# Kernel optimization log

Hardware: AMD Instinct MI355X
Metric: run time of the kernel (lower is better)

Reference implementation:

```python
import jax, jax.numpy as jnp
import numpy as np
from jax import lax

NUM_LAYERS = 128
SEQ_LEN = 256
H = 1  # hidden_size = input_size = 1


def setup_inputs() -> dict:
    key = jax.random.key(0)
    k = jax.random.split(key, 5)
    # PyTorch GRU init: U(-1/sqrt(H), 1/sqrt(H)) with H=1 -> U(-1, 1)
    u = lambda kk, shp: jax.random.uniform(kk, shp, jnp.float32, -1.0, 1.0)
    return {
        "x": jax.random.normal(k[0], (1, SEQ_LEN), jnp.float32),
        "w_ih": u(k[1], (NUM_LAYERS, 3 * H, H)),  # gates stacked [r, z, n]
        "w_hh": u(k[2], (NUM_LAYERS, 3 * H, H)),
        "b_ih": u(k[3], (NUM_LAYERS, 3 * H)),
        "b_hh": u(k[4], (NUM_LAYERS, 3 * H)),
    }


def _gru_stack(x_seq, w_ih, w_hh, b_ih, b_hh):
    # x_seq: [T, H]; params stacked over layers. PyTorch GRU equations, gate order r,z,n.
    def layer_step(seq, params):
        wi, wh, bi, bh = params  # [3H,H], [3H,H], [3H], [3H]

        def cell(h, xt):  # h: [H], xt: [H]
            gi = wi @ xt + bi  # [3H]
            gh = wh @ h + bh   # [3H]
            r = jax.nn.sigmoid(gi[0:H] + gh[0:H])
            z = jax.nn.sigmoid(gi[H:2 * H] + gh[H:2 * H])
            n = jnp.tanh(gi[2 * H:] + r * gh[2 * H:])
            h_new = (1.0 - z) * n + z * h
            return h_new, h_new

        h0 = jnp.zeros((H,), dtype=seq.dtype)
        _, out = lax.scan(cell, h0, seq)  # out: [T, H]
        return out, None

    out, _ = lax.scan(layer_step, x_seq, (w_ih, w_hh, b_ih, b_hh))
    return out


def reference(x, w_ih, w_hh, b_ih, b_hh):
    # x: [1, T] -> GRU input [T, H=1] (unbatched), encoder only (decoder unused in forward)
    seq = x.T  # [T, 1]
    out = _gru_stack(seq, w_ih, w_hh, b_ih, b_hh)  # [T, 1]
    return out.T  # [1, T]
```

## Files before the change

kernel.cpp:

```cpp
#include <hip/hip_runtime.h>

#define T_LEN 256
#define NG 25

__device__ __forceinline__ float ex2(float x) { return __builtin_amdgcn_exp2f(x); }
__device__ __forceinline__ float rcpf_(float x) { return __builtin_amdgcn_rcpf(x); }

__device__ __forceinline__ float dpp_shr1_fill(float fill, float v) {
    int f = __float_as_int(fill), i = __float_as_int(v);
    return __int_as_float(__builtin_amdgcn_update_dpp(f, i, 0x138, 0xF, 0xF, false));
}
__device__ __forceinline__ float dpp_shl1_fill(float fill, float v) {
    int f = __float_as_int(fill), i = __float_as_int(v);
    return __int_as_float(__builtin_amdgcn_update_dpp(f, i, 0x130, 0xF, 0xF, false));
}

__global__ __launch_bounds__(128, 1) void gru_stack_wavefront(
    const float* __restrict__ x,
    const float* __restrict__ w_ih,
    const float* __restrict__ w_hh,
    const float* __restrict__ b_ih,
    const float* __restrict__ b_hh,
    float* __restrict__ out)
{
    __shared__ float ring[2 * 64];
    __shared__ float sx[T_LEN];
    const int tid  = threadIdx.x;
    const int lane = tid & 63;
    const int wid  = tid >> 6;

    ring[tid] = 0.0f;
    sx[tid] = x[tid];
    sx[tid + 128] = x[tid + 128];

    const float L1 = -1.4426950408889634f;
    const float L2 = -2.8853900817779268f;

    const float wi_r = L1 * w_ih[3 * tid + 0], wh_r = L1 * w_hh[3 * tid + 0];
    const float b_r  = L1 * (b_ih[3 * tid + 0] + b_hh[3 * tid + 0]);
    const float wi_z = L1 * w_ih[3 * tid + 1], wh_z = L1 * w_hh[3 * tid + 1];
    const float b_z  = L1 * (b_ih[3 * tid + 1] + b_hh[3 * tid + 1]);
    const float wi_n = L2 * w_ih[3 * tid + 2], bi_n = L2 * b_ih[3 * tid + 2];
    const float wh_n = L2 * w_hh[3 * tid + 2], bh_n = L2 * b_hh[3 * tid + 2];

    float h = 0.0f;
    float c_r = b_r, c_z = b_z, g_n = bh_n;

    float pk[16];
    #pragma unroll
    for (int k = 0; k < 16; ++k) pk[k] = 0.0f;

    float ov = 0.0f;
    int t = -lane - 80 * wid - 1;

    const bool is_w1 = (wid == 1);
    float* ringw = &ring[wid * 64];

    __syncthreads();

    for (int g = 0; g < 9; ++g) {
        if (is_w1) {
            const int base = 16 * g - 17;
            #pragma unroll
            for (int k = 0; k < 16; ++k)
                pk[k] = ring[(base + k) & 63];
        } else {
            #pragma unroll
            for (int k = 0; k < 16; ++k)
                pk[k] = sx[16 * g + k];
        }

        #pragma unroll
        for (int k = 0; k < 16; ++k) {
            ++t;
            const bool valid = (unsigned)t < (unsigned)T_LEN;

            float in = dpp_shr1_fill(pk[k], h);

            float u_r  = fmaf(wi_r, in, c_r);
            float u_z  = fmaf(wi_z, in, c_z);
            float u_n0 = fmaf(wi_n, in, bi_n);
            float r  = rcpf_(1.0f + ex2(u_r));
            float Ez = ex2(u_z);
            Ez = valid ? Ez : 0.0f;
            float En = ex2(fmaf(r, g_n, u_n0));
            float t1  = 1.0f + En;
            float den = fmaf(Ez, t1, t1);
            float bb  = fmaf(-Ez, En, Ez);
            float num = fmaf(h, t1, bb);
            h = num * rcpf_(den);

            c_r = fmaf(wh_r, h, b_r);
            c_z = fmaf(wh_z, h, b_z);
            g_n = fmaf(wh_n, h, bh_n);

            ov = dpp_shl1_fill(h, ov);
        }
        ringw[(16 * g + 16 + lane) & 63] = ov;
        __syncthreads();
    }

    for (int g = 9; g < NG; ++g) {
        if (is_w1) {
            const int base = 16 * g - 17;
            #pragma unroll
            for (int k = 0; k < 16; ++k)
                pk[k] = ring[(base + k) & 63];
        } else {
            #pragma unroll
            for (int k = 0; k < 16; ++k)
                pk[k] = sx[(16 * g + k) & (T_LEN - 1)];
        }

        #pragma unroll
        for (int k = 0; k < 16; ++k) {
            float in = dpp_shr1_fill(pk[k], h);

            float u_r  = fmaf(wi_r, in, c_r);
            float u_z  = fmaf(wi_z, in, c_z);
            float u_n0 = fmaf(wi_n, in, bi_n);
            float r  = rcpf_(1.0f + ex2(u_r));
            float Ez = ex2(u_z);
            float En = ex2(fmaf(r, g_n, u_n0));
            float t1  = 1.0f + En;
            float den = fmaf(Ez, t1, t1);
            float bb  = fmaf(-Ez, En, Ez);
            float num = fmaf(h, t1, bb);
            h = num * rcpf_(den);

            c_r = fmaf(wh_r, h, b_r);
            c_z = fmaf(wh_z, h, b_z);
            g_n = fmaf(wh_n, h, bh_n);

            ov = dpp_shl1_fill(h, ov);

            if (k == 14) {
                if (is_w1 && (g & 3) == 0 && g >= 12)
                    out[16 * g - 192 + lane] = ov;
            }
        }
        ringw[(16 * g + 16 + lane) & 63] = ov;
        __syncthreads();
    }
}

extern "C" void kernel_launch(void* const* d_in, const int* in_sizes, int n_in,
                              void* d_out, int out_size, void* d_ws, size_t ws_size,
                              hipStream_t stream) {
    const float* x    = (const float*)d_in[0];
    const float* w_ih = (const float*)d_in[1];
    const float* w_hh = (const float*)d_in[2];
    const float* b_ih = (const float*)d_in[3];
    const float* b_hh = (const float*)d_in[4];
    float* out = (float*)d_out;

    gru_stack_wavefront<<<1, 128, 0, stream>>>(x, w_ih, w_hh, b_ih, b_hh, out);
}
```

Before: 84.43 us.

## Prefetch next LDS input group and shorten gate arithmetic critical path

Wave 0 now prefetches the next group of 16 x inputs from shared memory into a second register buffer during the current group's recurrence. Wave 1 loads the first ring entry of the next group one iteration early, so fewer LDS reads sit at the start of each group. The denominator is refactored to (1+Ez)(1+En), which lets 1+Ez be computed while the exp for n is still in flight. A custom barrier waits only on lgkmcnt before s_barrier. This costs extra registers and assumes the barrier semantics still make the ring writes visible.

```diff
diff --git a/kernel.cpp b/kernel.cpp
--- a/kernel.cpp
+++ b/kernel.cpp
@@ -13,6 +13,11 @@
 __device__ __forceinline__ float dpp_shl1_fill(float fill, float v) {
     int f = __float_as_int(fill), i = __float_as_int(v);
     return __int_as_float(__builtin_amdgcn_update_dpp(f, i, 0x130, 0xF, 0xF, false));
+}
+
+__device__ __forceinline__ void barrier_lds() {
+    asm volatile("s_waitcnt lgkmcnt(0)" ::: "memory");
+    __builtin_amdgcn_s_barrier();
 }
 
 __global__ __launch_bounds__(128, 1) void gru_stack_wavefront(
@@ -47,8 +52,10 @@
     float c_r = b_r, c_z = b_z, g_n = bh_n;
 
     float pk[16];
+    float pkn[16];
     #pragma unroll
-    for (int k = 0; k < 16; ++k) pk[k] = 0.0f;
+    for (int k = 0; k < 16; ++k) { pk[k] = 0.0f; pkn[k] = 0.0f; }
+    float pk0n = 0.0f;
 
     float ov = 0.0f;
     int t = -lane - 80 * wid - 1;
@@ -56,18 +63,25 @@
     const bool is_w1 = (wid == 1);
     float* ringw = &ring[wid * 64];
 
-    __syncthreads();
+    barrier_lds();
+
+    if (!is_w1) {
+        #pragma unroll
+        for (int k = 0; k < 16; ++k) pk[k] = sx[k];
+    }
 
     for (int g = 0; g < 9; ++g) {
         if (is_w1) {
             const int base = 16 * g - 17;
             #pragma unroll
-            for (int k = 0; k < 16; ++k)
+            for (int k = 1; k < 16; ++k)
                 pk[k] = ring[(base + k) & 63];
+            pk0n = ring[(base + 16) & 63];
         } else {
+            const int b2 = 16 * g + 16;
             #pragma unroll
             for (int k = 0; k < 16; ++k)
-                pk[k] = sx[16 * g + k];
+                pkn[k] = sx[b2 + k];
         }
 
         #pragma unroll
@@ -83,9 +97,10 @@
             float r  = rcpf_(1.0f + ex2(u_r));
             float Ez = ex2(u_z);
             Ez = valid ? Ez : 0.0f;
+            float az  = 1.0f + Ez;
             float En = ex2(fmaf(r, g_n, u_n0));
             float t1  = 1.0f + En;
-            float den = fmaf(Ez, t1, t1);
+            float den = fmaf(En, az, az);
             float bb  = fmaf(-Ez, En, Ez);
             float num = fmaf(h, t1, bb);
             h = num * rcpf_(den);
@@ -97,19 +112,27 @@
             ov = dpp_shl1_fill(h, ov);
         }
         ringw[(16 * g + 16 + lane) & 63] = ov;
-        __syncthreads();
+        if (is_w1) {
+            pk[0] = pk0n;
+        } else {
+            #pragma unroll
+            for (int k = 0; k < 16; ++k) pk[k] = pkn[k];
+        }
+        barrier_lds();
     }
 
     for (int g = 9; g < NG; ++g) {
         if (is_w1) {
             const int base = 16 * g - 17;
             #pragma unroll
-            for (int k = 0; k < 16; ++k)
+            for (int k = 1; k < 16; ++k)
                 pk[k] = ring[(base + k) & 63];
+            pk0n = ring[(base + 16) & 63];
         } else {
+            const int b2 = 16 * g + 16;
             #pragma unroll
             for (int k = 0; k < 16; ++k)
-                pk[k] = sx[(16 * g + k) & (T_LEN - 1)];
+                pkn[k] = sx[(b2 + k) & (T_LEN - 1)];
         }
 
         #pragma unroll
@@ -121,9 +144,10 @@
             float u_n0 = fmaf(wi_n, in, bi_n);
             float r  = rcpf_(1.0f + ex2(u_r));
             float Ez = ex2(u_z);
+            float az  = 1.0f + Ez;
             float En = ex2(fmaf(r, g_n, u_n0));
             float t1  = 1.0f + En;
-            float den = fmaf(Ez, t1, t1);
+            float den = fmaf(En, az, az);
             float bb  = fmaf(-Ez, En, Ez);
             float num = fmaf(h, t1, bb);
             h = num * rcpf_(den);
@@ -140,7 +164,13 @@
             }
         }
         ringw[(16 * g + 16 + lane) & 63] = ov;
-        __syncthreads();
+        if (is_w1) {
+            pk[0] = pk0n;
+        } else {
+            #pragma unroll
+            for (int k = 0; k < 16; ++k) pk[k] = pkn[k];
+        }
+        barrier_lds();
     }
 }
 
```

After: 86.63 us. +2.6%, slower.

## Run all 128 GRU layers in one wavefront with two layers per lane

Applied to the files above, without the earlier changes.

Replaces the two-wave layout, where each wave covers 64 layers and hands results across through an LDS ring with a __syncthreads per 16-step group, with a single 64-lane wave in which every lane computes two layers (A and B). Layer A's output reaches layer B through a DPP row-rotate and shift, so the LDS ring and all block barriers go away, and the schedule drops from 25 groups to 24. The cost is that each step now runs two dependent GRU cells back to back in one lane. Only the A and B chains are independent and can interleave to hide transcendental latency.

```diff
diff --git a/kernel.cpp b/kernel.cpp
--- a/kernel.cpp
+++ b/kernel.cpp
@@ -1,7 +1,7 @@
 #include <hip/hip_runtime.h>
 
 #define T_LEN 256
-#define NG 25
+#define NG 24
 
 __device__ __forceinline__ float ex2(float x) { return __builtin_amdgcn_exp2f(x); }
 __device__ __forceinline__ float rcpf_(float x) { return __builtin_amdgcn_rcpf(x); }
@@ -14,8 +14,12 @@
     int f = __float_as_int(fill), i = __float_as_int(v);
     return __int_as_float(__builtin_amdgcn_update_dpp(f, i, 0x130, 0xF, 0xF, false));
 }
+__device__ __forceinline__ float dpp_ror1(float v) {
+    int i = __float_as_int(v);
+    return __int_as_float(__builtin_amdgcn_update_dpp(i, i, 0x13C, 0xF, 0xF, false));
+}
 
-__global__ __launch_bounds__(128, 1) void gru_stack_wavefront(
+__global__ __launch_bounds__(64, 1) void gru_stack_wavefront(
     const float* __restrict__ x,
     const float* __restrict__ w_ih,
     const float* __restrict__ w_hh,
@@ -23,124 +27,145 @@
     const float* __restrict__ b_hh,
     float* __restrict__ out)
 {
-    __shared__ float ring[2 * 64];
     __shared__ float sx[T_LEN];
-    const int tid  = threadIdx.x;
-    const int lane = tid & 63;
-    const int wid  = tid >> 6;
+    const int lane = threadIdx.x;
 
-    ring[tid] = 0.0f;
-    sx[tid] = x[tid];
-    sx[tid + 128] = x[tid + 128];
+    sx[lane]       = x[lane];
+    sx[lane + 64]  = x[lane + 64];
+    sx[lane + 128] = x[lane + 128];
+    sx[lane + 192] = x[lane + 192];
 
     const float L1 = -1.4426950408889634f;
     const float L2 = -2.8853900817779268f;
 
-    const float wi_r = L1 * w_ih[3 * tid + 0], wh_r = L1 * w_hh[3 * tid + 0];
-    const float b_r  = L1 * (b_ih[3 * tid + 0] + b_hh[3 * tid + 0]);
-    const float wi_z = L1 * w_ih[3 * tid + 1], wh_z = L1 * w_hh[3 * tid + 1];
-    const float b_z  = L1 * (b_ih[3 * tid + 1] + b_hh[3 * tid + 1]);
-    const float wi_n = L2 * w_ih[3 * tid + 2], bi_n = L2 * b_ih[3 * tid + 2];
-    const float wh_n = L2 * w_hh[3 * tid + 2], bh_n = L2 * b_hh[3 * tid + 2];
+    const int la = lane;
+    const int lb = lane + 64;
 
-    float h = 0.0f;
-    float c_r = b_r, c_z = b_z, g_n = bh_n;
+    const float wi_rA = L1 * w_ih[3 * la + 0], wh_rA = L1 * w_hh[3 * la + 0];
+    const float b_rA  = L1 * (b_ih[3 * la + 0] + b_hh[3 * la + 0]);
+    const float wi_zA = L1 * w_ih[3 * la + 1], wh_zA = L1 * w_hh[3 * la + 1];
+    const float b_zA  = L1 * (b_ih[3 * la + 1] + b_hh[3 * la + 1]);
+    const float wi_nA = L2 * w_ih[3 * la + 2], bi_nA = L2 * b_ih[3 * la + 2];
+    const float wh_nA = L2 * w_hh[3 * la + 2], bh_nA = L2 * b_hh[3 * la + 2];
+
+    const float wi_rB = L1 * w_ih[3 * lb + 0], wh_rB = L1 * w_hh[3 * lb + 0];
+    const float b_rB  = L1 * (b_ih[3 * lb + 0] + b_hh[3 * lb + 0]);
+    const float wi_zB = L1 * w_ih[3 * lb + 1], wh_zB = L1 * w_hh[3 * lb + 1];
+    const float b_zB  = L1 * (b_ih[3 * lb + 1] + b_hh[3 * lb + 1]);
+    const float wi_nB = L2 * w_ih[3 * lb + 2], bi_nB = L2 * b_ih[3 * lb + 2];
+    const float wh_nB = L2 * w_hh[3 * lb + 2], bh_nB = L2 * b_hh[3 * lb + 2];
+
+    float hA = 0.0f, hB = 0.0f;
+    float c_rA = b_rA, c_zA = b_zA, g_nA = bh_nA;
+    float c_rB = b_rB, c_zB = b_zB, g_nB = bh_nB;
 
     float pk[16];
     #pragma unroll
     for (int k = 0; k < 16; ++k) pk[k] = 0.0f;
 
     float ov = 0.0f;
-    int t = -lane - 80 * wid - 1;
-
-    const bool is_w1 = (wid == 1);
-    float* ringw = &ring[wid * 64];
 
     __syncthreads();
 
-    for (int g = 0; g < 9; ++g) {
-        if (is_w1) {
-            const int base = 16 * g - 17;
-            #pragma unroll
-            for (int k = 0; k < 16; ++k)
-                pk[k] = ring[(base + k) & 63];
-        } else {
-            #pragma unroll
-            for (int k = 0; k < 16; ++k)
-                pk[k] = sx[16 * g + k];
-        }
+    for (int g = 0; g < 8; ++g) {
+        #pragma unroll
+        for (int k = 0; k < 16; ++k)
+            pk[k] = sx[16 * g + k];
 
         #pragma unroll
         for (int k = 0; k < 16; ++k) {
-            ++t;
-            const bool valid = (unsigned)t < (unsigned)T_LEN;
+            const int s = 16 * g + k;
+            const bool validA = (unsigned)(s - lane) < (unsigned)T_LEN;
+            const bool validB = (unsigned)(s - 64 - lane) < (unsigned)T_LEN;
 
-            float in = dpp_shr1_fill(pk[k], h);
+            float rA  = dpp_ror1(hA);
+            float inA = dpp_shr1_fill(pk[k], hA);
+            float inB = dpp_shr1_fill(rA, hB);
 
-            float u_r  = fmaf(wi_r, in, c_r);
-            float u_z  = fmaf(wi_z, in, c_z);
-            float u_n0 = fmaf(wi_n, in, bi_n);
-            float r  = rcpf_(1.0f + ex2(u_r));
-            float Ez = ex2(u_z);
-            Ez = valid ? Ez : 0.0f;
-            float En = ex2(fmaf(r, g_n, u_n0));
-            float t1  = 1.0f + En;
-            float den = fmaf(Ez, t1, t1);
-            float bb  = fmaf(-Ez, En, Ez);
-            float num = fmaf(h, t1, bb);
-            h = num * rcpf_(den);
+            float u_rA  = fmaf(wi_rA, inA, c_rA);
+            float u_zA  = fmaf(wi_zA, inA, c_zA);
+            float u_n0A = fmaf(wi_nA, inA, bi_nA);
+            float rrA = rcpf_(1.0f + ex2(u_rA));
+            float EzA = ex2(u_zA);
+            EzA = validA ? EzA : 0.0f;
+            float EnA = ex2(fmaf(rrA, g_nA, u_n0A));
+            float t1A  = 1.0f + EnA;
+            float denA = fmaf(EzA, t1A, t1A);
+            float bbA  = fmaf(-EzA, EnA, EzA);
+            float numA = fmaf(hA, t1A, bbA);
+            hA = numA * rcpf_(denA);
+            c_rA = fmaf(wh_rA, hA, b_rA);
+            c_zA = fmaf(wh_zA, hA, b_zA);
+            g_nA = fmaf(wh_nA, hA, bh_nA);
 
-            c_r = fmaf(wh_r, h, b_r);
-            c_z = fmaf(wh_z, h, b_z);
-            g_n = fmaf(wh_n, h, bh_n);
+            float u_rB  = fmaf(wi_rB, inB, c_rB);
+            float u_zB  = fmaf(wi_zB, inB, c_zB);
+            float u_n0B = fmaf(wi_nB, inB, bi_nB);
+            float rrB = rcpf_(1.0f + ex2(u_rB));
+            float EzB = ex2(u_zB);
+            EzB = validB ? EzB : 0.0f;
+            float EnB = ex2(fmaf(rrB, g_nB, u_n0B));
+            float t1B  = 1.0f + EnB;
+            float denB = fmaf(EzB, t1B, t1B);
+            float bbB  = fmaf(-EzB, EnB, EzB);
+            float numB = fmaf(hB, t1B, bbB);
+            hB = numB * rcpf_(denB);
+            c_rB = fmaf(wh_rB, hB, b_rB);
+            c_zB = fmaf(wh_zB, hB, b_zB);
+            g_nB = fmaf(wh_nB, hB, bh_nB);
 
-            ov = dpp_shl1_fill(h, ov);
+            ov = dpp_shl1_fill(hB, ov);
         }
-        ringw[(16 * g + 16 + lane) & 63] = ov;
-        __syncthreads();
     }
 
-    for (int g = 9; g < NG; ++g) {
-        if (is_w1) {
-            const int base = 16 * g - 17;
-            #pragma unroll
-            for (int k = 0; k < 16; ++k)
-                pk[k] = ring[(base + k) & 63];
-        } else {
-            #pragma unroll
-            for (int k = 0; k < 16; ++k)
-                pk[k] = sx[(16 * g + k) & (T_LEN - 1)];
-        }
+    for (int g = 8; g < NG; ++g) {
+        #pragma unroll
+        for (int k = 0; k < 16; ++k)
+            pk[k] = sx[(16 * g + k) & (T_LEN - 1)];
 
         #pragma unroll
         for (int k = 0; k < 16; ++k) {
-            float in = dpp_shr1_fill(pk[k], h);
+            float rA  = dpp_ror1(hA);
+            float inA = dpp_shr1_fill(pk[k], hA);
+            float inB = dpp_shr1_fill(rA, hB);
 
-            float u_r  = fmaf(wi_r, in, c_r);
-            float u_z  = fmaf(wi_z, in, c_z);
-            float u_n0 = fmaf(wi_n, in, bi_n);
-            float r  = rcpf_(1.0f + ex2(u_r));
-            float Ez = ex2(u_z);
-            float En = ex2(fmaf(r, g_n, u_n0));
-            float t1  = 1.0f + En;
-            float den = fmaf(Ez, t1, t1);
-            float bb  = fmaf(-Ez, En, Ez);
-            float num = fmaf(h, t1, bb);
-            h = num * rcpf_(den);
+            float u_rA  = fmaf(wi_rA, inA, c_rA);
+            float u_zA  = fmaf(wi_zA, inA, c_zA);
+            float u_n0A = fmaf(wi_nA, inA, bi_nA);
+            float rrA = rcpf_(1.0f + ex2(u_rA));
+            float EzA = ex2(u_zA);
+            float EnA = ex2(fmaf(rrA, g_nA, u_n0A));
+            float t1A  = 1.0f + EnA;
+            float denA = fmaf(EzA, t1A, t1A);
+            float bbA  = fmaf(-EzA, EnA, EzA);
+            float numA = fmaf(hA, t1A, bbA);
+            hA = numA * rcpf_(denA);
+            c_rA = fmaf(wh_rA, hA, b_rA);
+            c_zA = fmaf(wh_zA, hA, b_zA);
+            g_nA = fmaf(wh_nA, hA, bh_nA);
 
-            c_r = fmaf(wh_r, h, b_r);
-            c_z = fmaf(wh_z, h, b_z);
-            g_n = fmaf(wh_n, h, bh_n);
+            float u_rB  = fmaf(wi_rB, inB, c_rB);
+            float u_zB  = fmaf(wi_zB, inB, c_zB);
+            float u_n0B = fmaf(wi_nB, inB, bi_nB);
+            float rrB = rcpf_(1.0f + ex2(u_rB));
+            float EzB = ex2(u_zB);
+            float EnB = ex2(fmaf(rrB, g_nB, u_n0B));
+            float t1B  = 1.0f + EnB;
+            float denB = fmaf(EzB, t1B, t1B);
+            float bbB  = fmaf(-EzB, EnB, EzB);
+            float numB = fmaf(hB, t1B, bbB);
+            hB = numB * rcpf_(denB);
+            c_rB = fmaf(wh_rB, hB, b_rB);
+            c_zB = fmaf(wh_zB, hB, b_zB);
+            g_nB = fmaf(wh_nB, hB, bh_nB);
 
-            ov = dpp_shl1_fill(h, ov);
+            ov = dpp_shl1_fill(hB, ov);
 
             if (k == 14) {
-                if (is_w1 && (g & 3) == 0 && g >= 12)
-                    out[16 * g - 192 + lane] = ov;
+                if ((g & 3) == 3 && g >= 11)
+                    out[16 * g - 176 + lane] = ov;
             }
         }
-        ringw[(16 * g + 16 + lane) & 63] = ov;
-        __syncthreads();
     }
 }
 
@@ -154,5 +179,5 @@
     const float* b_hh = (const float*)d_in[4];
     float* out = (float*)d_out;
 
-    gru_stack_wavefront<<<1, 128, 0, stream>>>(x, w_ih, w_hh, b_ih, b_hh, out);
+    gru_stack_wavefront<<<1, 64, 0, stream>>>(x, w_ih, w_hh, b_ih, b_hh, out);
 }
```

Result: slower. 95.28 us (+12.9%).
